# Optimization experiments

Measured on AMD Instinct MI355X. Metric: run time of the kernel, lower is better.

Reference implementation:

```python
import jax, jax.numpy as jnp
import numpy as np

VOCAB_SIZE = 1024
EMBED_DIM = 64
Z_SHAPE = (64, 32, 32, EMBED_DIM)


def setup_inputs() -> dict:
    key = jax.random.key(0)
    kz, kc = jax.random.split(key)
    z = jax.random.normal(kz, Z_SHAPE, dtype=jnp.float32)
    codebook = jax.random.uniform(kc, (VOCAB_SIZE, EMBED_DIM), dtype=jnp.float32)
    return {"z": z, "codebook": codebook}


def reference(z, codebook):
    # Flatten all leading dims: [N, D]
    z_flat = jnp.reshape(z, (-1, EMBED_DIM))
    # Squared euclidean distance via expansion: |z|^2 + |c|^2 - 2 z.c
    d1 = jnp.sum(z_flat ** 2, axis=1, keepdims=True)      # [N, 1]
    d2 = jnp.sum(codebook ** 2, axis=1)                   # [V]
    d3 = 2.0 * jnp.dot(z_flat, codebook.T)                # [N, V]
    distances = d1 + d2 - d3                              # [N, V]
    tokens = jnp.argmin(distances, axis=1)                # [N]
    tokens = jnp.reshape(tokens, z.shape[:-1])            # [B, H, W]
    z_quantized = codebook[tokens]                        # [B, H, W, D]
    return (z_quantized, tokens, codebook)
```

## Files before the change

kernel.cpp:

```cpp
#include <hip/hip_runtime.h>
#include <float.h>

constexpr int D     = 64;
constexpr int V     = 1024;
constexpr int NROWS = 65536;
constexpr float MARGIN = 0.01f;

typedef _Float16 half8 __attribute__((ext_vector_type(8)));
typedef float    f32x4 __attribute__((ext_vector_type(4)));

__global__ __launch_bounds__(256) void vq_prep(
    const float* __restrict__ cb, _Float16* __restrict__ wsH,
    _Float16* __restrict__ wsL, float* __restrict__ c2,
    float* __restrict__ cbout, int* __restrict__ cnt) {
  const int t = blockIdx.x * 256 + threadIdx.x;
  if (t == 0) cnt[0] = 0;
#pragma unroll
  for (int i = 0; i < 16; ++i)
    ((float4*)cbout)[i * 1024 + t] = ((const float4*)cb)[i * 1024 + t];

  const int cw = t;
  const float* src = cb + (size_t)cw * D;
  float part = 0.f;
#pragma unroll
  for (int chunk = 0; chunk < 8; ++chunk) {
    float4 q0 = ((const float4*)(src + chunk * 8))[0];
    float4 q1 = ((const float4*)(src + chunk * 8))[1];
    float xs[8] = {q0.x, q0.y, q0.z, q0.w, q1.x, q1.y, q1.z, q1.w};
    half8 hh, hl;
#pragma unroll
    for (int e = 0; e < 8; ++e) {
      _Float16 hi = (_Float16)xs[e];
      hh[e] = hi;
      hl[e] = (_Float16)(xs[e] - (float)hi);
      part  = fmaf(xs[e], xs[e], part);
    }
    *(half8*)&wsH[((size_t)chunk * V + cw) * 8] = hh;
    *(half8*)&wsL[((size_t)chunk * V + cw) * 8] = hl;
  }
  c2[cw] = part;
}

__global__ __launch_bounds__(256, 6) void vq_screen(
    const float* __restrict__ z,
    const _Float16* __restrict__ wsH, const _Float16* __restrict__ wsL,
    const float* __restrict__ c2g,
    float* __restrict__ pB1, float* __restrict__ pB2, int* __restrict__ pI1) {
  __shared__ __align__(16) _Float16 sBh[8][64][8];
  __shared__ __align__(16) _Float16 sBl[8][64][8];
  __shared__ __align__(16) float sC2[64];

  const int tid  = threadIdx.x;
  const int lane = tid & 63;
  const int wv   = tid >> 6;
  const int l15  = lane & 15;
  const int quad = lane >> 4;
  const int half = blockIdx.x & 1;
  const int rowbase = (blockIdx.x >> 1) * 64 + wv * 16;

  half8 afh[2], afl[2];
  {
    const float* zr = z + (size_t)(rowbase + l15) * D;
#pragma unroll
    for (int h = 0; h < 2; ++h) {
      const float4* p = (const float4*)(zr + h * 32 + quad * 8);
      float4 q0 = p[0], q1 = p[1];
      float xs[8] = {q0.x, q0.y, q0.z, q0.w, q1.x, q1.y, q1.z, q1.w};
      half8 ah, al;
#pragma unroll
      for (int e = 0; e < 8; ++e) {
        _Float16 hi = (_Float16)xs[e];
        ah[e] = hi;
        al[e] = (_Float16)(xs[e] - (float)hi);
      }
      afh[h] = ah; afl[h] = al;
    }
  }

  float b1[4], b2[4]; int i1[4];
#pragma unroll
  for (int r = 0; r < 4; ++r) { b1[r] = FLT_MAX; b2[r] = FLT_MAX; i1[r] = 0; }

  for (int pp = 0; pp < 8; ++pp) {
    const int phase = half * 8 + pp;
    __syncthreads();
#pragma unroll
    for (int i = 0; i < 4; ++i) {
      const int idx   = i * 256 + tid;
      const int seg   = idx >> 6;
      const int off   = idx & 63;
      const int chunk = seg & 7;
      const _Float16* srcb = (seg < 8) ? wsH : wsL;
      const half8 v = *(const half8*)&srcb[((size_t)chunk * V + phase * 64 + off) * 8];
      if (seg < 8) *(half8*)&sBh[chunk][off][0] = v;
      else         *(half8*)&sBl[chunk][off][0] = v;
    }
    if (tid < 16) {
      float4 q = ((const float4*)(c2g + phase * 64))[tid];
      *(float4*)&sC2[tid * 4] = q;
    }
    __syncthreads();
#pragma unroll 2
    for (int tl = 0; tl < 4; ++tl) {
      const int cwl  = tl * 16 + l15;
      const int vcol = phase * 64 + cwl;
      const float c2v = sC2[cwl];
      half8 bh0 = *(const half8*)&sBh[quad][cwl][0];
      half8 bh1 = *(const half8*)&sBh[4 + quad][cwl][0];
      half8 bl0 = *(const half8*)&sBl[quad][cwl][0];
      half8 bl1 = *(const half8*)&sBl[4 + quad][cwl][0];
      f32x4 acc = {0.f, 0.f, 0.f, 0.f};
      acc = __builtin_amdgcn_mfma_f32_16x16x32_f16(afh[0], bh0, acc, 0, 0, 0);
      acc = __builtin_amdgcn_mfma_f32_16x16x32_f16(afh[1], bh1, acc, 0, 0, 0);
      acc = __builtin_amdgcn_mfma_f32_16x16x32_f16(afh[0], bl0, acc, 0, 0, 0);
      acc = __builtin_amdgcn_mfma_f32_16x16x32_f16(afh[1], bl1, acc, 0, 0, 0);
      acc = __builtin_amdgcn_mfma_f32_16x16x32_f16(afl[0], bh0, acc, 0, 0, 0);
      acc = __builtin_amdgcn_mfma_f32_16x16x32_f16(afl[1], bh1, acc, 0, 0, 0);
#pragma unroll
      for (int r = 0; r < 4; ++r) {
        float m0 = fmaf(-2.f, acc[r], c2v);
        bool  c0 = m0 < b1[r];
        b2[r] = fminf(b2[r], fmaxf(m0, b1[r]));
        b1[r] = c0 ? m0 : b1[r];
        i1[r] = c0 ? vcol : i1[r];
      }
    }
  }

#pragma unroll
  for (int r = 0; r < 4; ++r) {
    float v1 = b1[r], v2 = b2[r]; int ix = i1[r];
#pragma unroll
    for (int s = 1; s < 16; s <<= 1) {
      float ov1 = __shfl_xor(v1, s);
      float ov2 = __shfl_xor(v2, s);
      int   oix = __shfl_xor(ix, s);
      bool take = (ov1 < v1) || (ov1 == v1 && oix < ix);
      float worse = take ? v1 : ov1;
      v2 = fminf(fminf(v2, ov2), worse);
      v1 = take ? ov1 : v1;
      ix = take ? oix : ix;
    }
    b1[r] = v1; b2[r] = v2; i1[r] = ix;
  }

  if (l15 == 0) {
#pragma unroll
    for (int r = 0; r < 4; ++r) {
      const int grow = rowbase + quad * 4 + r;
      pB1[half * NROWS + grow] = b1[r];
      pB2[half * NROWS + grow] = b2[r];
      pI1[half * NROWS + grow] = i1[r];
    }
  }
}

__global__ __launch_bounds__(256) void vq_merge(
    const float* __restrict__ pB1, const float* __restrict__ pB2,
    const int* __restrict__ pI1, const float* __restrict__ cb,
    float* __restrict__ zq, float* __restrict__ tok,
    int* __restrict__ cnt, int* __restrict__ list) {
  __shared__ int sWin[256];
  const int tid = threadIdx.x;
  const int row = blockIdx.x * 256 + tid;

  float v1a = pB1[row];         float v2a = pB2[row];         int ixa = pI1[row];
  float v1b = pB1[NROWS + row]; float v2b = pB2[NROWS + row]; int ixb = pI1[NROWS + row];
  bool take  = (v1b < v1a) || (v1b == v1a && ixb < ixa);
  float worse = take ? v1a : v1b;
  float v2 = fminf(fminf(v2a, v2b), worse);
  float v1 = take ? v1b : v1a;
  int   ix = take ? ixb : ixa;

  tok[row]  = (float)ix;
  sWin[tid] = ix;
  if (v2 - v1 < MARGIN) {
    int s = atomicAdd(cnt, 1);
    list[s] = row;
  }
  __syncthreads();

  const int rb = blockIdx.x * 256;
#pragma unroll
  for (int i = 0; i < 16; ++i) {
    int cid = i * 256 + tid;
    int r = cid >> 4, seg = cid & 15;
    float4 val = *(const float4*)(cb + (size_t)sWin[r] * D + seg * 4);
    *(float4*)(zq + (size_t)(rb + r) * D + seg * 4) = val;
  }
}

__global__ __launch_bounds__(256) void vq_fallback(
    const float* __restrict__ z, const float* __restrict__ cb,
    const int* __restrict__ cnt, const int* __restrict__ list,
    float* __restrict__ zq, float* __restrict__ tok) {
  __shared__ float sv[256];
  __shared__ int   si[256];
  const int t = threadIdx.x;
  const int n = cnt[0];
  for (int it = blockIdx.x; it < n; it += gridDim.x) {
    int row = __builtin_amdgcn_readfirstlane(list[it]);
    const float* zr = z + (size_t)row * D;
    float zreg[D];
#pragma unroll
    for (int i = 0; i < D / 4; ++i) {
      float4 q = ((const float4*)zr)[i];
      zreg[4 * i] = q.x; zreg[4 * i + 1] = q.y; zreg[4 * i + 2] = q.z; zreg[4 * i + 3] = q.w;
    }
    float d1 = 0.f;
#pragma unroll
    for (int i = 0; i < D; ++i) d1 = fmaf(zreg[i], zreg[i], d1);
    float best = FLT_MAX; int bidx = 0;
    for (int c = 0; c < 4; ++c) {
      int v = t + 256 * c;
      const float* cp = cb + (size_t)v * D;
      float acc = 0.f, cc = 0.f;
#pragma unroll
      for (int dd = 0; dd < D; ++dd) {
        acc = fmaf(zreg[dd], cp[dd], acc);
        cc  = fmaf(cp[dd], cp[dd], cc);
      }
      float dist = (d1 + cc) - 2.f * acc;
      if (dist < best) { best = dist; bidx = v; }
    }
    sv[t] = best; si[t] = bidx;
    __syncthreads();
    for (int s = 128; s > 0; s >>= 1) {
      if (t < s) {
        float v2 = sv[t + s]; int i2 = si[t + s];
        if (v2 < sv[t] || (v2 == sv[t] && i2 < si[t])) { sv[t] = v2; si[t] = i2; }
      }
      __syncthreads();
    }
    int win = si[0];
    if (t == 0) tok[row] = (float)win;
    if (t < 16) {
      float4 q = ((const float4*)(cb + (size_t)win * D))[t];
      ((float4*)(zq + (size_t)row * D))[t] = q;
    }
    __syncthreads();
  }
}

extern "C" void kernel_launch(void* const* d_in, const int* in_sizes, int n_in,
                              void* d_out, int out_size, void* d_ws, size_t ws_size,
                              hipStream_t stream) {
  const float* z  = (const float*)d_in[0];
  const float* cb = (const float*)d_in[1];

  float* out = (float*)d_out;
  float* zq  = out;
  float* tok = out + (size_t)NROWS * D;
  float* cbo = tok + NROWS;

  char* wsb = (char*)d_ws;
  _Float16* wsH  = (_Float16*)(wsb + 0);
  _Float16* wsL  = (_Float16*)(wsb + 131072);
  float*    c2   = (float*)(wsb + 262144);
  int*      cnt  = (int*)(wsb + 266240);
  int*      list = (int*)(wsb + 266496);
  float*    pB1  = (float*)(wsb + 1048576);
  float*    pB2  = (float*)(wsb + 1572864);
  int*      pI1  = (int*)(wsb + 2097152);

  vq_prep<<<V / 256, 256, 0, stream>>>(cb, wsH, wsL, c2, cbo, cnt);
  vq_screen<<<2048, 256, 0, stream>>>(z, wsH, wsL, c2, pB1, pB2, pI1);
  vq_merge<<<NROWS / 256, 256, 0, stream>>>(pB1, pB2, pI1, cb, zq, tok, cnt, list);
  vq_fallback<<<1024, 256, 0, stream>>>(z, cb, cnt, list, zq, tok);
}
```

Baseline: 140.5 us.

## Keep codebook slice in registers per wave and split vocab into 16 partials

After: 170.8 us. +21.6%, slower.

```diff
diff --git a/kernel.cpp b/kernel.cpp
--- a/kernel.cpp
+++ b/kernel.cpp
@@ -41,81 +41,69 @@
   c2[cw] = part;
 }
 
-__global__ __launch_bounds__(256, 6) void vq_screen(
+__global__ __launch_bounds__(256) void vq_screen(
     const float* __restrict__ z,
     const _Float16* __restrict__ wsH, const _Float16* __restrict__ wsL,
     const float* __restrict__ c2g,
     float* __restrict__ pB1, float* __restrict__ pB2, int* __restrict__ pI1) {
-  __shared__ __align__(16) _Float16 sBh[8][64][8];
-  __shared__ __align__(16) _Float16 sBl[8][64][8];
-  __shared__ __align__(16) float sC2[64];
-
   const int tid  = threadIdx.x;
   const int lane = tid & 63;
   const int wv   = tid >> 6;
   const int l15  = lane & 15;
   const int quad = lane >> 4;
-  const int half = blockIdx.x & 1;
-  const int rowbase = (blockIdx.x >> 1) * 64 + wv * 16;
-
-  half8 afh[2], afl[2];
-  {
-    const float* zr = z + (size_t)(rowbase + l15) * D;
-#pragma unroll
-    for (int h = 0; h < 2; ++h) {
-      const float4* p = (const float4*)(zr + h * 32 + quad * 8);
-      float4 q0 = p[0], q1 = p[1];
-      float xs[8] = {q0.x, q0.y, q0.z, q0.w, q1.x, q1.y, q1.z, q1.w};
-      half8 ah, al;
-#pragma unroll
-      for (int e = 0; e < 8; ++e) {
-        _Float16 hi = (_Float16)xs[e];
-        ah[e] = hi;
-        al[e] = (_Float16)(xs[e] - (float)hi);
-      }
-      afh[h] = ah; afl[h] = al;
-    }
-  }
-
-  float b1[4], b2[4]; int i1[4];
-#pragma unroll
-  for (int r = 0; r < 4; ++r) { b1[r] = FLT_MAX; b2[r] = FLT_MAX; i1[r] = 0; }
-
-  for (int pp = 0; pp < 8; ++pp) {
-    const int phase = half * 8 + pp;
-    __syncthreads();
-#pragma unroll
-    for (int i = 0; i < 4; ++i) {
-      const int idx   = i * 256 + tid;
-      const int seg   = idx >> 6;
-      const int off   = idx & 63;
-      const int chunk = seg & 7;
-      const _Float16* srcb = (seg < 8) ? wsH : wsL;
-      const half8 v = *(const half8*)&srcb[((size_t)chunk * V + phase * 64 + off) * 8];
-      if (seg < 8) *(half8*)&sBh[chunk][off][0] = v;
-      else         *(half8*)&sBl[chunk][off][0] = v;
-    }
-    if (tid < 16) {
-      float4 q = ((const float4*)(c2g + phase * 64))[tid];
-      *(float4*)&sC2[tid * 4] = q;
-    }
-    __syncthreads();
-#pragma unroll 2
+  const int gw   = blockIdx.x * 4 + wv;
+  const int vg   = gw & 15;
+  const int rs   = gw >> 4;
+
+  half8 Bh0[4], Bh1[4], Bl0[4], Bl1[4];
+  float c2r[4];
+#pragma unroll
+  for (int tl = 0; tl < 4; ++tl) {
+    const int cw = vg * 64 + tl * 16 + l15;
+    Bh0[tl] = *(const half8*)&wsH[((size_t)quad       * V + cw) * 8];
+    Bh1[tl] = *(const half8*)&wsH[((size_t)(4 + quad) * V + cw) * 8];
+    Bl0[tl] = *(const half8*)&wsL[((size_t)quad       * V + cw) * 8];
+    Bl1[tl] = *(const half8*)&wsL[((size_t)(4 + quad) * V + cw) * 8];
+    c2r[tl] = c2g[cw];
+  }
+
+  for (int i = 0; i < 8; ++i) {
+    const int rowbase = rs * 128 + i * 16;
+
+    half8 afh[2], afl[2];
+    {
+      const float* zr = z + (size_t)(rowbase + l15) * D;
+#pragma unroll
+      for (int h = 0; h < 2; ++h) {
+        const float4* p = (const float4*)(zr + h * 32 + quad * 8);
+        float4 q0 = p[0], q1 = p[1];
+        float xs[8] = {q0.x, q0.y, q0.z, q0.w, q1.x, q1.y, q1.z, q1.w};
+        half8 ah, al;
+#pragma unroll
+        for (int e = 0; e < 8; ++e) {
+          _Float16 hi = (_Float16)xs[e];
+          ah[e] = hi;
+          al[e] = (_Float16)(xs[e] - (float)hi);
+        }
+        afh[h] = ah; afl[h] = al;
+      }
+    }
+
+    float b1[4], b2[4]; int i1[4];
+#pragma unroll
+    for (int r = 0; r < 4; ++r) { b1[r] = FLT_MAX; b2[r] = FLT_MAX; i1[r] = 0; }
+
+#pragma unroll
     for (int tl = 0; tl < 4; ++tl) {
-      const int cwl  = tl * 16 + l15;
-      const int vcol = phase * 64 + cwl;
-      const float c2v = sC2[cwl];
-      half8 bh0 = *(const half8*)&sBh[quad][cwl][0];
-      half8 bh1 = *(const half8*)&sBh[4 + quad][cwl][0];
-      half8 bl0 = *(const half8*)&sBl[quad][cwl][0];
-      half8 bl1 = *(const half8*)&sBl[4 + quad][cwl][0];
+      const int vcol = vg * 64 + tl * 16 + l15;
+      const float c2v = c2r[tl];
       f32x4 acc = {0.f, 0.f, 0.f, 0.f};
-      acc = __builtin_amdgcn_mfma_f32_16x16x32_f16(afh[0], bh0, acc, 0, 0, 0);
-      acc = __builtin_amdgcn_mfma_f32_16x16x32_f16(afh[1], bh1, acc, 0, 0, 0);
-      acc = __builtin_amdgcn_mfma_f32_16x16x32_f16(afh[0], bl0, acc, 0, 0, 0);
-      acc = __builtin_amdgcn_mfma_f32_16x16x32_f16(afh[1], bl1, acc, 0, 0, 0);
-      acc = __builtin_amdgcn_mfma_f32_16x16x32_f16(afl[0], bh0, acc, 0, 0, 0);
-      acc = __builtin_amdgcn_mfma_f32_16x16x32_f16(afl[1], bh1, acc, 0, 0, 0);
+      acc = __builtin_amdgcn_mfma_f32_16x16x32_f16(afh[0], Bh0[tl], acc, 0, 0, 0);
+      acc = __builtin_amdgcn_mfma_f32_16x16x32_f16(afh[1], Bh1[tl], acc, 0, 0, 0);
+      acc = __builtin_amdgcn_mfma_f32_16x16x32_f16(afh[0], Bl0[tl], acc, 0, 0, 0);
+      acc = __builtin_amdgcn_mfma_f32_16x16x32_f16(afh[1], Bl1[tl], acc, 0, 0, 0);
+      acc = __builtin_amdgcn_mfma_f32_16x16x32_f16(afl[0], Bh0[tl], acc, 0, 0, 0);
+      acc = __builtin_amdgcn_mfma_f32_16x16x32_f16(afl[1], Bh1[tl], acc, 0, 0, 0);
 #pragma unroll
       for (int r = 0; r < 4; ++r) {
         float m0 = fmaf(-2.f, acc[r], c2v);
@@ -125,32 +113,32 @@
         i1[r] = c0 ? vcol : i1[r];
       }
     }
-  }
-
-#pragma unroll
-  for (int r = 0; r < 4; ++r) {
-    float v1 = b1[r], v2 = b2[r]; int ix = i1[r];
-#pragma unroll
-    for (int s = 1; s < 16; s <<= 1) {
-      float ov1 = __shfl_xor(v1, s);
-      float ov2 = __shfl_xor(v2, s);
-      int   oix = __shfl_xor(ix, s);
-      bool take = (ov1 < v1) || (ov1 == v1 && oix < ix);
-      float worse = take ? v1 : ov1;
-      v2 = fminf(fminf(v2, ov2), worse);
-      v1 = take ? ov1 : v1;
-      ix = take ? oix : ix;
-    }
-    b1[r] = v1; b2[r] = v2; i1[r] = ix;
-  }
-
-  if (l15 == 0) {
+
 #pragma unroll
     for (int r = 0; r < 4; ++r) {
-      const int grow = rowbase + quad * 4 + r;
-      pB1[half * NROWS + grow] = b1[r];
-      pB2[half * NROWS + grow] = b2[r];
-      pI1[half * NROWS + grow] = i1[r];
+      float v1 = b1[r], v2 = b2[r]; int ix = i1[r];
+#pragma unroll
+      for (int s = 1; s < 16; s <<= 1) {
+        float ov1 = __shfl_xor(v1, s);
+        float ov2 = __shfl_xor(v2, s);
+        int   oix = __shfl_xor(ix, s);
+        bool take = (ov1 < v1) || (ov1 == v1 && oix < ix);
+        float worse = take ? v1 : ov1;
+        v2 = fminf(fminf(v2, ov2), worse);
+        v1 = take ? ov1 : v1;
+        ix = take ? oix : ix;
+      }
+      b1[r] = v1; b2[r] = v2; i1[r] = ix;
+    }
+
+    if (l15 == 0) {
+#pragma unroll
+      for (int r = 0; r < 4; ++r) {
+        const int grow = rowbase + quad * 4 + r;
+        pB1[(size_t)vg * NROWS + grow] = b1[r];
+        pB2[(size_t)vg * NROWS + grow] = b2[r];
+        pI1[(size_t)vg * NROWS + grow] = i1[r];
+      }
     }
   }
 }
@@ -164,13 +152,18 @@
   const int tid = threadIdx.x;
   const int row = blockIdx.x * 256 + tid;
 
-  float v1a = pB1[row];         float v2a = pB2[row];         int ixa = pI1[row];
-  float v1b = pB1[NROWS + row]; float v2b = pB2[NROWS + row]; int ixb = pI1[NROWS + row];
-  bool take  = (v1b < v1a) || (v1b == v1a && ixb < ixa);
-  float worse = take ? v1a : v1b;
-  float v2 = fminf(fminf(v2a, v2b), worse);
-  float v1 = take ? v1b : v1a;
-  int   ix = take ? ixb : ixa;
+  float v1 = pB1[row], v2 = pB2[row]; int ix = pI1[row];
+#pragma unroll
+  for (int h = 1; h < 16; ++h) {
+    float w1 = pB1[(size_t)h * NROWS + row];
+    float w2 = pB2[(size_t)h * NROWS + row];
+    int   jx = pI1[(size_t)h * NROWS + row];
+    bool take  = (w1 < v1) || (w1 == v1 && jx < ix);
+    float worse = take ? v1 : w1;
+    v2 = fminf(fminf(v2, w2), worse);
+    v1 = take ? w1 : v1;
+    ix = take ? jx : ix;
+  }
 
   tok[row]  = (float)ix;
   sWin[tid] = ix;
@@ -259,9 +252,9 @@
   float*    c2   = (float*)(wsb + 262144);
   int*      cnt  = (int*)(wsb + 266240);
   int*      list = (int*)(wsb + 266496);
-  float*    pB1  = (float*)(wsb + 1048576);
-  float*    pB2  = (float*)(wsb + 1572864);
-  int*      pI1  = (int*)(wsb + 2097152);
+  float*    pB1  = (float*)(wsb + (size_t)4  * 1024 * 1024);
+  float*    pB2  = (float*)(wsb + (size_t)8  * 1024 * 1024);
+  int*      pI1  = (int*)(wsb + (size_t)12 * 1024 * 1024);
 
   vq_prep<<<V / 256, 256, 0, stream>>>(cb, wsH, wsL, c2, cbo, cnt);
   vq_screen<<<2048, 256, 0, stream>>>(z, wsH, wsL, c2, pB1, pB2, pI1);
```
